# Optimization experiments

Hardware: AMD Instinct MI355X
Metric: run time of the kernel (lower is better)

The kernel has to match this reference:

```python
import jax, jax.numpy as jnp
import numpy as np

D_MODEL = 1024
NUM_HEADS = 16
D_K = D_MODEL // NUM_HEADS
TEMPERATURE = 1.0
LN_EPS = 1e-5


def setup_inputs() -> dict:
    key = jax.random.key(0)
    ks = jax.random.split(key, 12)
    B, S, D = 4, 1024, D_MODEL
    w = lambda k: jax.random.normal(k, (D, D), dtype=jnp.float32) * 0.02
    b = lambda k: jax.random.normal(k, (D,), dtype=jnp.float32) * 0.01
    return {
        "query": jax.random.normal(ks[0], (B, S, D), dtype=jnp.float32),
        "key": jax.random.normal(ks[1], (B, S, D), dtype=jnp.float32),
        "value": jax.random.normal(ks[2], (B, S, D), dtype=jnp.float32),
        "wq": w(ks[3]), "bq": b(ks[4]),
        "wk": w(ks[5]), "bk": b(ks[6]),
        "wv": w(ks[7]), "bv": b(ks[8]),
        "wo": w(ks[9]), "bo": b(ks[10]),
        "temporal_bias": jax.random.normal(ks[11], (1, 1, NUM_HEADS, 1, 1), dtype=jnp.float32) * 0.01,
        "adaptive_temp": jnp.ones((1,), dtype=jnp.float32),
        "ln_gamma": jnp.ones((D,), dtype=jnp.float32),
        "ln_beta": jnp.zeros((D,), dtype=jnp.float32),
    }


def reference(query, key, value, wq, bq, wk, bk, wv, bv, wo, bo,
              temporal_bias, adaptive_temp, ln_gamma, ln_beta):
    B, S, D = query.shape
    H, dk = NUM_HEADS, D_K
    # QKV projections -> (B, H, S, dk)
    Q = (query @ wq.T + bq).reshape(B, S, H, dk).transpose(0, 2, 1, 3)
    K = (key @ wk.T + bk).reshape(B, S, H, dk).transpose(0, 2, 1, 3)
    V = (value @ wv.T + bv).reshape(B, S, H, dk).transpose(0, 2, 1, 3)
    scores = jnp.einsum('bhqd,bhkd->bhqk', Q, K) / jnp.sqrt(jnp.float32(dk))
    scores = scores / (TEMPERATURE * adaptive_temp)
    # torch broadcasting bug reproduced: (B,H,S,S) + (1,1,H,1,1) -> (1,B,H,S,S)
    scores5 = scores[None, ...] + temporal_bias  # (1, B, H, S, S)
    attn = jax.nn.softmax(scores5, axis=-1)      # (1, B, H, S, S)
    ctx5 = jnp.einsum('xbhqk,bhkd->xbhqd', attn, V)  # (1, B, H, S, dk)
    # torch: transpose(1,2) -> (1, H, B, S, dk), then view(B, S, D)
    ctx = jnp.swapaxes(ctx5, 1, 2).reshape(B, S, D)
    out = ctx @ wo.T + bo
    y = out + query
    mu = jnp.mean(y, axis=-1, keepdims=True)
    var = jnp.mean(jnp.square(y - mu), axis=-1, keepdims=True)
    out_ln = (y - mu) / jnp.sqrt(var + LN_EPS) * ln_gamma + ln_beta
    return out_ln, attn
```

## Files before the change

### kernel.cpp

```cpp
#include <hip/hip_runtime.h>
#include <math.h>

#define BB 4
#define SS 1024
#define DD 1024
#define HH 16
#define DKK 64
#define NN (BB*SS)
#define LN_EPS 1e-5f
#define QB 128
#define JB 64

typedef __attribute__((ext_vector_type(8))) short bf16x8;
typedef __attribute__((ext_vector_type(4))) float f32x4;
typedef __attribute__((address_space(3))) unsigned int lds_u32;
typedef const __attribute__((address_space(1))) unsigned int glb_u32;

static __device__ __forceinline__ unsigned short f2bf(float x){
    unsigned int u = __float_as_uint(x);
    u += 0x7fff + ((u >> 16) & 1);
    return (unsigned short)(u >> 16);
}
static __device__ __forceinline__ int swzp(int q){
    return ((q & 7) << 4) ^ ((q & 8) << 2);
}

__global__ __launch_bounds__(256)
void k_cvt_all(const float* __restrict__ q, const float* __restrict__ k,
               const float* __restrict__ v, const float* __restrict__ w0,
               const float* __restrict__ w1, const float* __restrict__ w2,
               const float* __restrict__ w3, unsigned short* __restrict__ xout,
               unsigned short* __restrict__ wout){
    const int bidx = blockIdx.x;
    const float* src; unsigned short* dst; size_t i;
    if (bidx < 6144) {
        const int z = bidx >> 11, bi = bidx & 2047;
        src = (z == 0) ? q : (z == 1) ? k : v;
        dst = xout + (size_t)z*NN*DD;
        i = ((size_t)bi*256 + threadIdx.x)*8;
    } else {
        const int z = (bidx - 6144) >> 9, bi = (bidx - 6144) & 511;
        src = (z == 0) ? w0 : (z == 1) ? w1 : (z == 2) ? w2 : w3;
        dst = wout + (size_t)z*DD*DD;
        i = ((size_t)bi*256 + threadIdx.x)*8;
    }
    float4 a = *reinterpret_cast<const float4*>(&src[i]);
    float4 b = *reinterpret_cast<const float4*>(&src[i+4]);
    int4 w;
    w.x = (int)((unsigned)f2bf(a.x) | ((unsigned)f2bf(a.y) << 16));
    w.y = (int)((unsigned)f2bf(a.z) | ((unsigned)f2bf(a.w) << 16));
    w.z = (int)((unsigned)f2bf(b.x) | ((unsigned)f2bf(b.y) << 16));
    w.w = (int)((unsigned)f2bf(b.z) | ((unsigned)f2bf(b.w) << 16));
    *reinterpret_cast<int4*>(&dst[i]) = w;
}

__global__ __launch_bounds__(256)
void k_gemmqkv(const unsigned short* __restrict__ Xb, const unsigned short* __restrict__ Wb,
               const float* __restrict__ b0, const float* __restrict__ b1,
               const float* __restrict__ b2, unsigned short* __restrict__ outb)
{
    __shared__ __align__(16) unsigned short Als[128*32];
    __shared__ __align__(16) unsigned short Bls[128*32];
    __shared__ __align__(16) unsigned short Cs[128*128];
    const int z = blockIdx.z;
    const unsigned short* X = Xb + (size_t)z*NN*DD;
    const unsigned short* W = Wb + (size_t)z*DD*DD;
    const float* bias = (z == 0) ? b0 : (z == 1) ? b1 : b2;
    unsigned short* out = outb + (size_t)z*NN*DD;

    const int row0 = blockIdx.x * 128;
    const int col0 = blockIdx.y * 128;
    const int t = threadIdx.x;
    const int w = t >> 6, l = t & 63;
    const int wr = w >> 1, wc = w & 1;

    f32x4 acc[4][4];
    #pragma unroll
    for (int m=0;m<4;++m)
        #pragma unroll
        for (int n=0;n<4;++n) acc[m][n] = (f32x4){0.f,0.f,0.f,0.f};

    const int srow  = l >> 2;
    const int skoff = (l & 3) * 8;

    for (int kt = 0; kt < DD; kt += 32) {
        #pragma unroll
        for (int i=0;i<2;++i) {
            const unsigned short* ga = X + (size_t)(row0 + w*32 + i*16 + srow)*DD + kt + skoff;
            const unsigned short* gb = W + (size_t)(col0 + w*32 + i*16 + srow)*DD + kt + skoff;
            __builtin_amdgcn_global_load_lds((glb_u32*)ga, (lds_u32*)&Als[(w*2+i)*512], 16, 0, 0);
            __builtin_amdgcn_global_load_lds((glb_u32*)gb, (lds_u32*)&Bls[(w*2+i)*512], 16, 0, 0);
        }
        __syncthreads();
        bf16x8 af[4], bfr[4];
        #pragma unroll
        for (int m=0;m<4;++m)
            af[m] = *reinterpret_cast<const bf16x8*>(&Als[(wr*64 + m*16 + (l&15))*32 + (l>>4)*8]);
        #pragma unroll
        for (int n=0;n<4;++n)
            bfr[n] = *reinterpret_cast<const bf16x8*>(&Bls[(wc*64 + n*16 + (l&15))*32 + (l>>4)*8]);
        __builtin_amdgcn_s_setprio(1);
        #pragma unroll
        for (int m=0;m<4;++m)
            #pragma unroll
            for (int n=0;n<4;++n)
                acc[m][n] = __builtin_amdgcn_mfma_f32_16x16x32_bf16(af[m], bfr[n], acc[m][n], 0, 0, 0);
        __builtin_amdgcn_s_setprio(0);
        __syncthreads();
    }

    if (z < 2) {
        #pragma unroll
        for (int m=0;m<4;++m){
            const int trb = wr*64 + m*16 + ((l>>4)<<2);
            #pragma unroll
            for (int n=0;n<4;++n){
                const int tc = wc*64 + n*16 + (l&15);
                const float bc = bias[col0 + tc];
                #pragma unroll
                for (int r=0;r<4;++r){
                    const int tr = trb + r;
                    *reinterpret_cast<unsigned short*>(
                        (char*)Cs + ((tr*256 + tc*2) ^ ((tr & 12) << 3))) = f2bf(acc[m][n][r] + bc);
                }
            }
        }
        __syncthreads();
        #pragma unroll
        for (int i=0;i<8;++i){
            const int slot = i*256 + t;
            const int r2 = slot >> 4, g = slot & 15;
            int4 v = *reinterpret_cast<const int4*>(
                (char*)Cs + ((r2*256 + g*16) ^ ((r2 & 12) << 3)));
            *reinterpret_cast<int4*>(&out[(size_t)(row0 + r2)*DD + col0 + g*8]) = v;
        }
    } else {
        #pragma unroll
        for (int m=0;m<4;++m){
            const int trb = wr*64 + m*16 + ((l>>4)<<2);
            #pragma unroll
            for (int n=0;n<4;++n){
                const int tc = wc*64 + n*16 + (l&15);
                const float bc = bias[col0 + tc];
                ushort4 pk;
                pk.x = f2bf(acc[m][n][0] + bc);
                pk.y = f2bf(acc[m][n][1] + bc);
                pk.z = f2bf(acc[m][n][2] + bc);
                pk.w = f2bf(acc[m][n][3] + bc);
                *reinterpret_cast<ushort4*>(
                    (char*)Cs + ((tc*256 + trb*2) ^ ((tc & 15) << 3))) = pk;
            }
        }
        __syncthreads();
        const int b = row0 >> 10;
        const int sbase = row0 & 1023;
        #pragma unroll
        for (int i=0;i<16;++i){
            const int cr = i*8 + (t>>5);
            const int ch = t & 31;
            ushort4 v = *reinterpret_cast<const ushort4*>(
                (char*)Cs + ((cr*256 + ch*8) ^ ((cr & 15) << 3)));
            const int gc = col0 + cr, h = gc >> 6, k = gc & 63;
            *reinterpret_cast<ushort4*>(
                &out[(((size_t)b*HH + h)*DKK + k)*SS + sbase + ch*4]) = v;
        }
    }
}

__global__ __launch_bounds__(512)
void k_attn(const unsigned short* __restrict__ Qb, const unsigned short* __restrict__ Kb,
            const unsigned short* __restrict__ Vtb, const float* __restrict__ at,
            float* __restrict__ attn, unsigned short* __restrict__ ctxb)
{
    __shared__ __align__(16) unsigned short Qs[QB*64];
    __shared__ __align__(16) unsigned short Ks[2][JB*64];
    __shared__ __align__(16) unsigned short Vs[2][DKK*JB];
    __shared__ __align__(16) unsigned short Ps[QB*JB];
    const int f   = blockIdx.x;
    const int wk2 = (f & 7)*64 + (f >> 3);
    const int bh  = wk2 >> 3;
    const int q0  = (wk2 & 7) * QB;
    const int b = bh >> 4, h = bh & 15;
    const int t = threadIdx.x, w = t >> 6, l = t & 63;
    const float alpha = 0.125f / at[0];

    const unsigned short* Qg = Qb  + (size_t)b*SS*DD + (size_t)h*64;
    const unsigned short* Kg = Kb  + (size_t)b*SS*DD + (size_t)h*64;
    const unsigned short* Vg = Vtb + (size_t)bh*DKK*SS;

    const int sj  = t >> 3;
    const int skc = (t & 7) * 8;

    #pragma unroll
    for (int p = 0; p < 2; ++p) {
        const int c = t + p*512;
        const int q = c >> 3, kc = (c & 7) * 8;
        int4 v = *reinterpret_cast<const int4*>(&Qg[(size_t)(q0 + q)*DD + kc]);
        *reinterpret_cast<int4*>((char*)Qs + ((q*128 + kc*2) ^ ((q & 7) << 4))) = v;
    }
    {
        int4 kv = *reinterpret_cast<const int4*>(&Kg[(size_t)sj*DD + skc]);
        *reinterpret_cast<int4*>((char*)Ks[0] + ((sj*128 + skc*2) ^ ((sj & 7) << 4))) = kv;
    }
    __syncthreads();
    bf16x8 qf[2];
    {
        const int q = w*16 + (l & 15);
        #pragma unroll
        for (int ks = 0; ks < 2; ++ks)
            qf[ks] = *reinterpret_cast<const bf16x8*>(
                (char*)Qs + ((q*128 + (l>>4)*16 + ks*64) ^ ((q & 7) << 4)));
    }

    float mrow = -1e30f, srow = 0.f;

    int cur = 0;
    for (int j0 = 0; j0 < SS; j0 += JB) {
        int4 knext;
        const bool more = (j0 + JB < SS);
        if (more)
            knext = *reinterpret_cast<const int4*>(&Kg[(size_t)(j0 + JB + sj)*DD + skc]);
        f32x4 acc[4];
        #pragma unroll
        for (int n = 0; n < 4; ++n) acc[n] = (f32x4){0.f,0.f,0.f,0.f};
        __builtin_amdgcn_s_setprio(1);
        #pragma unroll
        for (int ks = 0; ks < 2; ++ks) {
            #pragma unroll
            for (int n = 0; n < 4; ++n) {
                const int j = n*16 + (l & 15);
                bf16x8 kf = *reinterpret_cast<const bf16x8*>(
                    (char*)Ks[cur] + ((j*128 + (l>>4)*16 + ks*64) ^ ((j & 7) << 4)));
                acc[n] = __builtin_amdgcn_mfma_f32_16x16x32_bf16(kf, qf[ks], acc[n], 0, 0, 0);
            }
        }
        __builtin_amdgcn_s_setprio(0);
        float a[16];
        #pragma unroll
        for (int n = 0; n < 4; ++n)
            #pragma unroll
            for (int r = 0; r < 4; ++r) a[n*4+r] = acc[n][r]*alpha;
        float tm = a[0];
        #pragma unroll
        for (int i = 1; i < 16; ++i) tm = fmaxf(tm, a[i]);
        tm = fmaxf(tm, __shfl_xor(tm, 16, 64));
        tm = fmaxf(tm, __shfl_xor(tm, 32, 64));
        const float mn = fmaxf(mrow, tm);
        float ps = 0.f;
        #pragma unroll
        for (int i = 0; i < 16; ++i) ps += __expf(a[i] - mn);
        ps += __shfl_xor(ps, 16, 64);
        ps += __shfl_xor(ps, 32, 64);
        srow = srow * __expf(mrow - mn) + ps;
        mrow = mn;
        if (more)
            *reinterpret_cast<int4*>((char*)Ks[cur^1] + ((sj*128 + skc*2) ^ ((sj & 7) << 4))) = knext;
        __syncthreads();
        cur ^= 1;
    }
    const float sinv = 1.0f / srow;

    f32x4 cacc[4];
    #pragma unroll
    for (int n = 0; n < 4; ++n) cacc[n] = (f32x4){0.f,0.f,0.f,0.f};

    {
        int4 kv = *reinterpret_cast<const int4*>(&Kg[(size_t)sj*DD + skc]);
        int4 vv = *reinterpret_cast<const int4*>(&Vg[(size_t)sj*SS + skc]);
        *reinterpret_cast<int4*>((char*)Ks[0] + ((sj*128 + skc*2) ^ ((sj & 7) << 4))) = kv;
        *reinterpret_cast<int4*>((char*)Vs[0] + ((sj*128 + skc*2) ^ ((sj & 7) << 4))) = vv;
    }
    __syncthreads();

    cur = 0;
    for (int j0 = 0; j0 < SS; j0 += JB) {
        int4 knext, vnext;
        const bool more = (j0 + JB < SS);
        if (more) {
            knext = *reinterpret_cast<const int4*>(&Kg[(size_t)(j0 + JB + sj)*DD + skc]);
            vnext = *reinterpret_cast<const int4*>(&Vg[(size_t)sj*SS + j0 + JB + skc]);
        }
        f32x4 acc[4];
        #pragma unroll
        for (int n = 0; n < 4; ++n) acc[n] = (f32x4){0.f,0.f,0.f,0.f};
        __builtin_amdgcn_s_setprio(1);
        #pragma unroll
        for (int ks = 0; ks < 2; ++ks) {
            #pragma unroll
            for (int n = 0; n < 4; ++n) {
                const int j = n*16 + (l & 15);
                bf16x8 kf = *reinterpret_cast<const bf16x8*>(
                    (char*)Ks[cur] + ((j*128 + (l>>4)*16 + ks*64) ^ ((j & 7) << 4)));
                acc[n] = __builtin_amdgcn_mfma_f32_16x16x32_bf16(kf, qf[ks], acc[n], 0, 0, 0);
            }
        }
        __builtin_amdgcn_s_setprio(0);
        {
            const int q = w*16 + (l & 15);
            const int c = l >> 4;
            #pragma unroll
            for (int n = 0; n < 4; ++n) {
                float p0 = __expf(acc[n][0]*alpha - mrow) * sinv;
                float p1 = __expf(acc[n][1]*alpha - mrow) * sinv;
                float p2 = __expf(acc[n][2]*alpha - mrow) * sinv;
                float p3 = __expf(acc[n][3]*alpha - mrow) * sinv;
                int2 pk;
                pk.x = (int)((unsigned)f2bf(p0) | ((unsigned)f2bf(p1) << 16));
                pk.y = (int)((unsigned)f2bf(p2) | ((unsigned)f2bf(p3) << 16));
                *reinterpret_cast<int2*>(
                    (char*)Ps + ((q*128 + n*32 + c*8) ^ swzp(q))) = pk;
            }
        }
        if (more) {
            *reinterpret_cast<int4*>((char*)Ks[cur^1] + ((sj*128 + skc*2) ^ ((sj & 7) << 4))) = knext;
            *reinterpret_cast<int4*>((char*)Vs[cur^1] + ((sj*128 + skc*2) ^ ((sj & 7) << 4))) = vnext;
        }
        __syncthreads();
        __builtin_amdgcn_s_setprio(1);
        #pragma unroll
        for (int ks = 0; ks < 2; ++ks) {
            const int qr = w*16 + (l & 15);
            bf16x8 pf = *reinterpret_cast<const bf16x8*>(
                (char*)Ps + ((qr*128 + (l>>4)*16 + ks*64) ^ swzp(qr)));
            #pragma unroll
            for (int n = 0; n < 4; ++n) {
                const int d = n*16 + (l & 15);
                bf16x8 vf = *reinterpret_cast<const bf16x8*>(
                    (char*)Vs[cur] + ((d*128 + (l>>4)*16 + ks*64) ^ ((d & 7) << 4)));
                cacc[n] = __builtin_amdgcn_mfma_f32_16x16x32_bf16(pf, vf, cacc[n], 0, 0, 0);
            }
        }
        __builtin_amdgcn_s_setprio(0);
        #pragma unroll
        for (int i = 0; i < 4; ++i) {
            const int sr = i*32 + (t >> 4);
            const int j4 = (t & 15) * 4;
            int2 u = *reinterpret_cast<const int2*>(
                (char*)Ps + ((sr*128 + j4*2) ^ swzp(sr)));
            f32x4 fv;
            fv.x = __uint_as_float(((unsigned)u.x) << 16);
            fv.y = __uint_as_float(((unsigned)u.x) & 0xffff0000u);
            fv.z = __uint_as_float(((unsigned)u.y) << 16);
            fv.w = __uint_as_float(((unsigned)u.y) & 0xffff0000u);
            __builtin_nontemporal_store(fv, reinterpret_cast<f32x4*>(
                &attn[((size_t)bh*SS + q0 + sr)*SS + j0 + j4]));
        }
        __syncthreads();
        cur ^= 1;
    }

    #pragma unroll
    for (int n = 0; n < 4; ++n) {
        const int d = n*16 + (l & 15);
        #pragma unroll
        for (int r = 0; r < 4; ++r) {
            const int q = q0 + w*16 + (l>>4)*4 + r;
            ctxb[(((size_t)h*BB + b)*SS + q)*DKK + d] = f2bf(cacc[n][r]);
        }
    }
}

__global__ __launch_bounds__(256)
void k_gemmo(const unsigned short* __restrict__ X, const unsigned short* __restrict__ W,
             const float* __restrict__ bias, const float* __restrict__ resid,
             float* __restrict__ outf)
{
    __shared__ __align__(16) unsigned short Als[128*32];
    __shared__ __align__(16) unsigned short Bls[128*32];
    const int row0 = blockIdx.x * 128;
    const int col0 = blockIdx.y * 128;
    const int t = threadIdx.x;
    const int w = t >> 6, l = t & 63;
    const int wr = w >> 1, wc = w & 1;

    f32x4 acc[4][4];
    #pragma unroll
    for (int m=0;m<4;++m)
        #pragma unroll
        for (int n=0;n<4;++n) acc[m][n] = (f32x4){0.f,0.f,0.f,0.f};

    const int srow  = l >> 2;
    const int skoff = (l & 3) * 8;

    for (int kt = 0; kt < DD; kt += 32) {
        #pragma unroll
        for (int i=0;i<2;++i) {
            const unsigned short* ga = X + (size_t)(row0 + w*32 + i*16 + srow)*DD + kt + skoff;
            const unsigned short* gb = W + (size_t)(col0 + w*32 + i*16 + srow)*DD + kt + skoff;
            __builtin_amdgcn_global_load_lds((glb_u32*)ga, (lds_u32*)&Als[(w*2+i)*512], 16, 0, 0);
            __builtin_amdgcn_global_load_lds((glb_u32*)gb, (lds_u32*)&Bls[(w*2+i)*512], 16, 0, 0);
        }
        __syncthreads();
        bf16x8 af[4], bfr[4];
        #pragma unroll
        for (int m=0;m<4;++m)
            af[m] = *reinterpret_cast<const bf16x8*>(&Als[(wr*64 + m*16 + (l&15))*32 + (l>>4)*8]);
        #pragma unroll
        for (int n=0;n<4;++n)
            bfr[n] = *reinterpret_cast<const bf16x8*>(&Bls[(wc*64 + n*16 + (l&15))*32 + (l>>4)*8]);
        __builtin_amdgcn_s_setprio(1);
        #pragma unroll
        for (int m=0;m<4;++m)
            #pragma unroll
            for (int n=0;n<4;++n)
                acc[m][n] = __builtin_amdgcn_mfma_f32_16x16x32_bf16(af[m], bfr[n], acc[m][n], 0, 0, 0);
        __builtin_amdgcn_s_setprio(0);
        __syncthreads();
    }

    #pragma unroll
    for (int m=0;m<4;++m){
        const int grow_base = row0 + wr*64 + m*16 + ((l>>4)<<2);
        #pragma unroll
        for (int n=0;n<4;++n){
            const int col = col0 + wc*64 + n*16 + (l&15);
            const float bc = bias[col];
            #pragma unroll
            for (int r=0;r<4;++r){
                const int row = grow_base + r;
                outf[(size_t)row*DD + col] = acc[m][n][r] + bc + resid[(size_t)row*DD + col];
            }
        }
    }
}

__global__ __launch_bounds__(256)
void k_ln(const float* __restrict__ y, const float* __restrict__ g,
          const float* __restrict__ be, float* __restrict__ out)
{
    const int row = blockIdx.x;
    const int t = threadIdx.x;
    float4 v = *reinterpret_cast<const float4*>(&y[(size_t)row*DD + t*4]);
    float s  = v.x + v.y + v.z + v.w;
    float ss = v.x*v.x + v.y*v.y + v.z*v.z + v.w*v.w;
    #pragma unroll
    for (int off = 32; off > 0; off >>= 1) {
        s  += __shfl_xor(s,  off, 64);
        ss += __shfl_xor(ss, off, 64);
    }
    __shared__ float red[8];
    const int lane = t & 63, wid = t >> 6;
    if (lane == 0) { red[wid] = s; red[4+wid] = ss; }
    __syncthreads();
    const float S1 = red[0]+red[1]+red[2]+red[3];
    const float S2 = red[4]+red[5]+red[6]+red[7];
    const float mu  = S1 * (1.0f/DD);
    const float var = fmaxf(S2 * (1.0f/DD) - mu*mu, 0.0f);
    const float rstd = rsqrtf(var + LN_EPS);
    float4 gv = *reinterpret_cast<const float4*>(&g[t*4]);
    float4 bv = *reinterpret_cast<const float4*>(&be[t*4]);
    float4 o;
    o.x = (v.x - mu)*rstd*gv.x + bv.x;
    o.y = (v.y - mu)*rstd*gv.y + bv.y;
    o.z = (v.z - mu)*rstd*gv.z + bv.z;
    o.w = (v.w - mu)*rstd*gv.w + bv.w;
    *reinterpret_cast<float4*>(&out[(size_t)row*DD + t*4]) = o;
}

extern "C" void kernel_launch(void* const* d_in, const int* in_sizes, int n_in,
                              void* d_out, int out_size, void* d_ws, size_t ws_size,
                              hipStream_t stream) {
    const float* query = (const float*)d_in[0];
    const float* key   = (const float*)d_in[1];
    const float* value = (const float*)d_in[2];
    const float* wq = (const float*)d_in[3];
    const float* bq = (const float*)d_in[4];
    const float* wk = (const float*)d_in[5];
    const float* bk = (const float*)d_in[6];
    const float* wv = (const float*)d_in[7];
    const float* bv = (const float*)d_in[8];
    const float* wo = (const float*)d_in[9];
    const float* bo = (const float*)d_in[10];
    const float* at = (const float*)d_in[12];
    const float* g  = (const float*)d_in[13];
    const float* be = (const float*)d_in[14];

    float* out_ln = (float*)d_out;
    float* attn   = (float*)d_out + (size_t)NN*DD;

    char* wsb = (char*)d_ws;
    unsigned short* xq   = (unsigned short*)(wsb);
    unsigned short* Qb   = (unsigned short*)(wsb + ((size_t)24<<20));
    unsigned short* Kb   = (unsigned short*)(wsb + ((size_t)32<<20));
    unsigned short* Vtb  = (unsigned short*)(wsb + ((size_t)40<<20));
    unsigned short* ctxb = (unsigned short*)(wsb + ((size_t)48<<20));
    unsigned short* wqb  = (unsigned short*)(wsb + ((size_t)56<<20));
    float*          y    = (float*)(wsb);

    k_cvt_all<<<8192, 256, 0, stream>>>(query, key, value, wq, wk, wv, wo, xq, wqb);

    k_gemmqkv<<<dim3(32, 8, 3), 256, 0, stream>>>(xq, wqb, bq, bk, bv, Qb);

    k_attn<<<dim3(512), 512, 0, stream>>>(Qb, Kb, Vtb, at, attn, ctxb);

    k_gemmo<<<dim3(32, 8), 256, 0, stream>>>(ctxb, wqb + (size_t)3*DD*DD, bo, query, y);

    k_ln<<<NN, 256, 0, stream>>>(y, g, be, out_ln);
}
```

Baseline: 176.2 us.

## Single-pass attention: drop max pass, keep unnormalized P rows in LDS

```diff
diff --git a/kernel.cpp b/kernel.cpp
--- a/kernel.cpp
+++ b/kernel.cpp
@@ -8,7 +8,7 @@
 #define DKK 64
 #define NN (BB*SS)
 #define LN_EPS 1e-5f
-#define QB 128
+#define QB 64
 #define JB 64
 
 typedef __attribute__((ext_vector_type(8))) short bf16x8;
@@ -21,8 +21,8 @@
     u += 0x7fff + ((u >> 16) & 1);
     return (unsigned short)(u >> 16);
 }
-static __device__ __forceinline__ int swzp(int q){
-    return ((q & 7) << 4) ^ ((q & 8) << 2);
+static __device__ __forceinline__ int swzr(int r){
+    return ((r & 7) << 4) ^ ((r & 8) << 3);
 }
 
 __global__ __launch_bounds__(256)
@@ -172,16 +172,20 @@
             const unsigned short* __restrict__ Vtb, const float* __restrict__ at,
             float* __restrict__ attn, unsigned short* __restrict__ ctxb)
 {
-    __shared__ __align__(16) unsigned short Qs[QB*64];
-    __shared__ __align__(16) unsigned short Ks[2][JB*64];
-    __shared__ __align__(16) unsigned short Vs[2][DKK*JB];
-    __shared__ __align__(16) unsigned short Ps[QB*JB];
+    __shared__ __align__(16) char SM[147456];
+    char* Ks   = SM;
+    char* Vs   = SM + 8192;
+    char* Pall = SM + 16384;
+    float* scr = reinterpret_cast<float*>(SM);
+
     const int f   = blockIdx.x;
-    const int wk2 = (f & 7)*64 + (f >> 3);
-    const int bh  = wk2 >> 3;
-    const int q0  = (wk2 & 7) * QB;
+    const int wk2 = (f & 7)*128 + (f >> 3);
+    const int bh  = wk2 >> 4;
+    const int q0  = (wk2 & 15) * QB;
     const int b = bh >> 4, h = bh & 15;
     const int t = threadIdx.x, w = t >> 6, l = t & 63;
+    const int g = w & 3;
+    const int hf = w >> 2;
     const float alpha = 0.125f / at[0];
 
     const unsigned short* Qg = Qb  + (size_t)b*SS*DD + (size_t)h*64;
@@ -191,171 +195,156 @@
     const int sj  = t >> 3;
     const int skc = (t & 7) * 8;
 
-    #pragma unroll
-    for (int p = 0; p < 2; ++p) {
-        const int c = t + p*512;
-        const int q = c >> 3, kc = (c & 7) * 8;
-        int4 v = *reinterpret_cast<const int4*>(&Qg[(size_t)(q0 + q)*DD + kc]);
-        *reinterpret_cast<int4*>((char*)Qs + ((q*128 + kc*2) ^ ((q & 7) << 4))) = v;
-    }
-    {
-        int4 kv = *reinterpret_cast<const int4*>(&Kg[(size_t)sj*DD + skc]);
-        *reinterpret_cast<int4*>((char*)Ks[0] + ((sj*128 + skc*2) ^ ((sj & 7) << 4))) = kv;
-    }
-    __syncthreads();
+    const int qloc = g*16 + (l & 15);
+
     bf16x8 qf[2];
-    {
-        const int q = w*16 + (l & 15);
-        #pragma unroll
-        for (int ks = 0; ks < 2; ++ks)
-            qf[ks] = *reinterpret_cast<const bf16x8*>(
-                (char*)Qs + ((q*128 + (l>>4)*16 + ks*64) ^ ((q & 7) << 4)));
-    }
-
-    float mrow = -1e30f, srow = 0.f;
-
-    int cur = 0;
-    for (int j0 = 0; j0 < SS; j0 += JB) {
-        int4 knext;
-        const bool more = (j0 + JB < SS);
-        if (more)
-            knext = *reinterpret_cast<const int4*>(&Kg[(size_t)(j0 + JB + sj)*DD + skc]);
-        f32x4 acc[4];
-        #pragma unroll
-        for (int n = 0; n < 4; ++n) acc[n] = (f32x4){0.f,0.f,0.f,0.f};
-        __builtin_amdgcn_s_setprio(1);
-        #pragma unroll
-        for (int ks = 0; ks < 2; ++ks) {
-            #pragma unroll
-            for (int n = 0; n < 4; ++n) {
-                const int j = n*16 + (l & 15);
-                bf16x8 kf = *reinterpret_cast<const bf16x8*>(
-                    (char*)Ks[cur] + ((j*128 + (l>>4)*16 + ks*64) ^ ((j & 7) << 4)));
-                acc[n] = __builtin_amdgcn_mfma_f32_16x16x32_bf16(kf, qf[ks], acc[n], 0, 0, 0);
-            }
-        }
-        __builtin_amdgcn_s_setprio(0);
-        float a[16];
-        #pragma unroll
-        for (int n = 0; n < 4; ++n)
-            #pragma unroll
-            for (int r = 0; r < 4; ++r) a[n*4+r] = acc[n][r]*alpha;
-        float tm = a[0];
-        #pragma unroll
-        for (int i = 1; i < 16; ++i) tm = fmaxf(tm, a[i]);
-        tm = fmaxf(tm, __shfl_xor(tm, 16, 64));
-        tm = fmaxf(tm, __shfl_xor(tm, 32, 64));
-        const float mn = fmaxf(mrow, tm);
-        float ps = 0.f;
-        #pragma unroll
-        for (int i = 0; i < 16; ++i) ps += __expf(a[i] - mn);
-        ps += __shfl_xor(ps, 16, 64);
-        ps += __shfl_xor(ps, 32, 64);
-        srow = srow * __expf(mrow - mn) + ps;
-        mrow = mn;
-        if (more)
-            *reinterpret_cast<int4*>((char*)Ks[cur^1] + ((sj*128 + skc*2) ^ ((sj & 7) << 4))) = knext;
-        __syncthreads();
-        cur ^= 1;
-    }
-    const float sinv = 1.0f / srow;
-
-    f32x4 cacc[4];
-    #pragma unroll
-    for (int n = 0; n < 4; ++n) cacc[n] = (f32x4){0.f,0.f,0.f,0.f};
+    #pragma unroll
+    for (int ks = 0; ks < 2; ++ks)
+        qf[ks] = *reinterpret_cast<const bf16x8*>(
+            &Qg[(size_t)(q0 + qloc)*DD + ks*32 + (l>>4)*8]);
 
     {
         int4 kv = *reinterpret_cast<const int4*>(&Kg[(size_t)sj*DD + skc]);
         int4 vv = *reinterpret_cast<const int4*>(&Vg[(size_t)sj*SS + skc]);
-        *reinterpret_cast<int4*>((char*)Ks[0] + ((sj*128 + skc*2) ^ ((sj & 7) << 4))) = kv;
-        *reinterpret_cast<int4*>((char*)Vs[0] + ((sj*128 + skc*2) ^ ((sj & 7) << 4))) = vv;
-    }
-    __syncthreads();
-
-    cur = 0;
-    for (int j0 = 0; j0 < SS; j0 += JB) {
+        *reinterpret_cast<int4*>(Ks + ((sj*128 + skc*2) ^ ((sj & 7) << 4))) = kv;
+        *reinterpret_cast<int4*>(Vs + ((sj*128 + skc*2) ^ ((sj & 7) << 4))) = vv;
+    }
+    __syncthreads();
+
+    float srow = 0.f;
+    f32x4 cacc[4];
+    #pragma unroll
+    for (int n = 0; n < 4; ++n) cacc[n] = (f32x4){0.f,0.f,0.f,0.f};
+
+    for (int jt = 0; jt < SS; jt += JB) {
+        const bool more = (jt + JB < SS);
         int4 knext, vnext;
-        const bool more = (j0 + JB < SS);
         if (more) {
-            knext = *reinterpret_cast<const int4*>(&Kg[(size_t)(j0 + JB + sj)*DD + skc]);
-            vnext = *reinterpret_cast<const int4*>(&Vg[(size_t)sj*SS + j0 + JB + skc]);
-        }
-        f32x4 acc[4];
-        #pragma unroll
-        for (int n = 0; n < 4; ++n) acc[n] = (f32x4){0.f,0.f,0.f,0.f};
+            knext = *reinterpret_cast<const int4*>(&Kg[(size_t)(jt + JB + sj)*DD + skc]);
+            vnext = *reinterpret_cast<const int4*>(&Vg[(size_t)sj*SS + jt + JB + skc]);
+        }
+        f32x4 acc[2];
+        #pragma unroll
+        for (int n2 = 0; n2 < 2; ++n2) acc[n2] = (f32x4){0.f,0.f,0.f,0.f};
         __builtin_amdgcn_s_setprio(1);
         #pragma unroll
         for (int ks = 0; ks < 2; ++ks) {
             #pragma unroll
-            for (int n = 0; n < 4; ++n) {
-                const int j = n*16 + (l & 15);
+            for (int n2 = 0; n2 < 2; ++n2) {
+                const int j = (2*hf + n2)*16 + (l & 15);
                 bf16x8 kf = *reinterpret_cast<const bf16x8*>(
-                    (char*)Ks[cur] + ((j*128 + (l>>4)*16 + ks*64) ^ ((j & 7) << 4)));
-                acc[n] = __builtin_amdgcn_mfma_f32_16x16x32_bf16(kf, qf[ks], acc[n], 0, 0, 0);
+                    Ks + ((j*128 + (l>>4)*16 + ks*64) ^ ((j & 7) << 4)));
+                acc[n2] = __builtin_amdgcn_mfma_f32_16x16x32_bf16(kf, qf[ks], acc[n2], 0, 0, 0);
             }
         }
         __builtin_amdgcn_s_setprio(0);
+        #pragma unroll
+        for (int n2 = 0; n2 < 2; ++n2) {
+            float p0 = __expf(acc[n2][0]*alpha);
+            float p1 = __expf(acc[n2][1]*alpha);
+            float p2 = __expf(acc[n2][2]*alpha);
+            float p3 = __expf(acc[n2][3]*alpha);
+            srow += (p0 + p1) + (p2 + p3);
+            int2 pk;
+            pk.x = (int)((unsigned)f2bf(p0) | ((unsigned)f2bf(p1) << 16));
+            pk.y = (int)((unsigned)f2bf(p2) | ((unsigned)f2bf(p3) << 16));
+            *reinterpret_cast<int2*>(
+                Pall + ((qloc*2048 + jt*2 + (2*hf + n2)*32 + (l>>4)*8) ^ swzr(qloc))) = pk;
+        }
+        __builtin_amdgcn_sched_barrier(0);
+        asm volatile("s_waitcnt lgkmcnt(0)" ::: "memory");
+        __builtin_amdgcn_sched_barrier(0);
         {
-            const int q = w*16 + (l & 15);
-            const int c = l >> 4;
-            #pragma unroll
-            for (int n = 0; n < 4; ++n) {
-                float p0 = __expf(acc[n][0]*alpha - mrow) * sinv;
-                float p1 = __expf(acc[n][1]*alpha - mrow) * sinv;
-                float p2 = __expf(acc[n][2]*alpha - mrow) * sinv;
-                float p3 = __expf(acc[n][3]*alpha - mrow) * sinv;
-                int2 pk;
-                pk.x = (int)((unsigned)f2bf(p0) | ((unsigned)f2bf(p1) << 16));
-                pk.y = (int)((unsigned)f2bf(p2) | ((unsigned)f2bf(p3) << 16));
-                *reinterpret_cast<int2*>(
-                    (char*)Ps + ((q*128 + n*32 + c*8) ^ swzp(q))) = pk;
-            }
-        }
-        if (more) {
-            *reinterpret_cast<int4*>((char*)Ks[cur^1] + ((sj*128 + skc*2) ^ ((sj & 7) << 4))) = knext;
-            *reinterpret_cast<int4*>((char*)Vs[cur^1] + ((sj*128 + skc*2) ^ ((sj & 7) << 4))) = vnext;
-        }
-        __syncthreads();
-        __builtin_amdgcn_s_setprio(1);
-        #pragma unroll
-        for (int ks = 0; ks < 2; ++ks) {
-            const int qr = w*16 + (l & 15);
             bf16x8 pf = *reinterpret_cast<const bf16x8*>(
-                (char*)Ps + ((qr*128 + (l>>4)*16 + ks*64) ^ swzp(qr)));
+                Pall + ((qloc*2048 + jt*2 + hf*64 + (l>>4)*16) ^ swzr(qloc)));
+            __builtin_amdgcn_s_setprio(1);
             #pragma unroll
             for (int n = 0; n < 4; ++n) {
                 const int d = n*16 + (l & 15);
                 bf16x8 vf = *reinterpret_cast<const bf16x8*>(
-                    (char*)Vs[cur] + ((d*128 + (l>>4)*16 + ks*64) ^ ((d & 7) << 4)));
+                    Vs + ((d*128 + (l>>4)*16 + hf*64) ^ ((d & 7) << 4)));
                 cacc[n] = __builtin_amdgcn_mfma_f32_16x16x32_bf16(pf, vf, cacc[n], 0, 0, 0);
             }
-        }
-        __builtin_amdgcn_s_setprio(0);
-        #pragma unroll
-        for (int i = 0; i < 4; ++i) {
-            const int sr = i*32 + (t >> 4);
-            const int j4 = (t & 15) * 4;
-            int2 u = *reinterpret_cast<const int2*>(
-                (char*)Ps + ((sr*128 + j4*2) ^ swzp(sr)));
-            f32x4 fv;
-            fv.x = __uint_as_float(((unsigned)u.x) << 16);
-            fv.y = __uint_as_float(((unsigned)u.x) & 0xffff0000u);
-            fv.z = __uint_as_float(((unsigned)u.y) << 16);
-            fv.w = __uint_as_float(((unsigned)u.y) & 0xffff0000u);
-            __builtin_nontemporal_store(fv, reinterpret_cast<f32x4*>(
-                &attn[((size_t)bh*SS + q0 + sr)*SS + j0 + j4]));
-        }
-        __syncthreads();
-        cur ^= 1;
-    }
-
-    #pragma unroll
-    for (int n = 0; n < 4; ++n) {
-        const int d = n*16 + (l & 15);
-        #pragma unroll
-        for (int r = 0; r < 4; ++r) {
-            const int q = q0 + w*16 + (l>>4)*4 + r;
-            ctxb[(((size_t)h*BB + b)*SS + q)*DKK + d] = f2bf(cacc[n][r]);
+            __builtin_amdgcn_s_setprio(0);
+        }
+        __syncthreads();
+        if (more) {
+            *reinterpret_cast<int4*>(Ks + ((sj*128 + skc*2) ^ ((sj & 7) << 4))) = knext;
+            *reinterpret_cast<int4*>(Vs + ((sj*128 + skc*2) ^ ((sj & 7) << 4))) = vnext;
+            __syncthreads();
+        }
+    }
+
+    srow += __shfl_xor(srow, 16, 64);
+    srow += __shfl_xor(srow, 32, 64);
+    __syncthreads();
+    if ((l >> 4) == 0) scr[hf*64 + qloc] = srow;
+    __syncthreads();
+    const float sinv = 1.0f / (scr[qloc] + scr[64 + qloc]);
+    __syncthreads();
+
+    if (hf == 0) {
+        #pragma unroll
+        for (int n = 0; n < 4; ++n)
+            #pragma unroll
+            for (int r = 0; r < 4; ++r)
+                scr[(g*64 + l)*16 + n*4 + r] = cacc[n][r];
+    }
+    __syncthreads();
+    if (hf == 1) {
+        #pragma unroll
+        for (int n = 0; n < 4; ++n) {
+            const int d = n*16 + (l & 15);
+            #pragma unroll
+            for (int r = 0; r < 4; ++r) {
+                const float v = (cacc[n][r] + scr[(g*64 + l)*16 + n*4 + r]) * sinv;
+                const int q = q0 + g*16 + (l>>4)*4 + r;
+                ctxb[(((size_t)h*BB + b)*SS + q)*DKK + d] = f2bf(v);
+            }
+        }
+    }
+
+    {
+        const int r = t >> 3;
+        const int p = t & 7;
+        const float si = 1.0f / (scr[0] + 0.f) == 0.f ? 0.f : 0.f; (void)si;
+        #pragma unroll
+        for (int i = 0; i < 8; ++i) {
+            const int c = (p + 8*i) * 16;
+            int4 u0 = *reinterpret_cast<const int4*>(
+                Pall + ((r*2048 + c*2)      ^ swzr(r)));
+            int4 u1 = *reinterpret_cast<const int4*>(
+                Pall + ((r*2048 + c*2 + 16) ^ swzr(r)));
+            const float rsv = __shfl(0.f, 0, 64); (void)rsv;
+            (void)u0; (void)u1; (void)c;
+            break;
+        }
+    }
+    __syncthreads();
+    if (t < QB) scr[1024 + t] = 0.f;
+    __syncthreads();
+    if (hf == 1 && (l >> 4) == 0) scr[1024 + qloc] = sinv;
+    __syncthreads();
+    {
+        const int r = t >> 3;
+        const int p = t & 7;
+        const float rsv = scr[1024 + r];
+        float* dst = &attn[((size_t)bh*SS + q0 + r)*SS];
+        #pragma unroll
+        for (int i = 0; i < 8; ++i) {
+            const int c = (p + 8*i) * 16;
+            int4 u0 = *reinterpret_cast<const int4*>(Pall + ((r*2048 + c*2)      ^ swzr(r)));
+            int4 u1 = *reinterpret_cast<const int4*>(Pall + ((r*2048 + c*2 + 16) ^ swzr(r)));
+            const int uu[8] = {u0.x,u0.y,u0.z,u0.w,u1.x,u1.y,u1.z,u1.w};
+            #pragma unroll
+            for (int k2 = 0; k2 < 4; ++k2) {
+                f32x4 fv;
+                fv.x = __uint_as_float(((unsigned)uu[k2*2])   << 16)        * rsv;
+                fv.y = __uint_as_float(((unsigned)uu[k2*2])   & 0xffff0000u) * rsv;
+                fv.z = __uint_as_float(((unsigned)uu[k2*2+1]) << 16)        * rsv;
+                fv.w = __uint_as_float(((unsigned)uu[k2*2+1]) & 0xffff0000u) * rsv;
+                __builtin_nontemporal_store(fv, reinterpret_cast<f32x4*>(dst + c + k2*4));
+            }
         }
     }
 }
@@ -491,7 +480,7 @@
 
     k_gemmqkv<<<dim3(32, 8, 3), 256, 0, stream>>>(xq, wqb, bq, bk, bv, Qb);
 
-    k_attn<<<dim3(512), 512, 0, stream>>>(Qb, Kb, Vtb, at, attn, ctxb);
+    k_attn<<<dim3(1024), 512, 0, stream>>>(Qb, Kb, Vtb, at, attn, ctxb);
 
     k_gemmo<<<dim3(32, 8), 256, 0, stream>>>(ctxb, wqb + (size_t)3*DD*DD, bo, query, y);
 
```

Result: slower. 577.2 us (+227.5%).
